# Optimization experiments

Hardware: AMD Instinct MI355X
Metric: run time of the kernel (lower is better)

The kernel has to match this reference:

```python
import jax, jax.numpy as jnp
import numpy as np

OUT_FEATURES = 11008
IN_FEATURES = 4096
GROUP_SIZE = 128
N_GROUPS = IN_FEATURES // GROUP_SIZE


def setup_inputs() -> dict:
    key = jax.random.key(0)
    k1, k2, k3 = jax.random.split(key, 3)
    x = jax.random.normal(k1, (4, 2048, IN_FEATURES), dtype=jnp.float32)
    # random packed bytes: every uint8 pattern decodes to a valid (low, high) nibble pair
    weight_packed = jax.random.randint(k2, (OUT_FEATURES, IN_FEATURES // 2), 0, 256, dtype=jnp.int32)
    # positive per-group scales (typical magnitude ~ max|w|/7)
    scales = jax.random.uniform(k3, (OUT_FEATURES, N_GROUPS), dtype=jnp.float32, minval=1e-3, maxval=0.05)
    return {"x": x, "weight_packed": weight_packed, "scales": scales}


def _dequant(weight_packed, scales):
    # unpack nibbles: low nibble = even index, high nibble = odd index; stored as (q+8)
    even = (weight_packed & 15) - 8                    # [O, I/2]
    odd = ((weight_packed >> 4) & 15) - 8              # [O, I/2]
    w_q = jnp.stack([even, odd], axis=-1).reshape(OUT_FEATURES, IN_FEATURES)  # interleave
    w = w_q.astype(jnp.float32).reshape(OUT_FEATURES, N_GROUPS, GROUP_SIZE)
    w = w * scales[:, :, None]                          # group-wise dequant
    return w.reshape(OUT_FEATURES, IN_FEATURES)


def reference(x, weight_packed, scales):
    w = _dequant(weight_packed, scales).astype(x.dtype)  # [O, I]
    # F.linear(x, w) = x @ w.T
    return jnp.einsum('bsi,oi->bso', x, w)
```

## Files before the change

kernel.cpp:

```cpp
#include <hip/hip_runtime.h>
#include <stdint.h>

#define K_DIM 4096
#define N_GROUPS 32

#define BM 128
#define BN 128
#define BK 32

#define BM8 256
#define BN8 256
#define BK8 64
#define NT8 (K_DIM / BK8)

typedef __attribute__((ext_vector_type(4))) float f32x4;
typedef __attribute__((ext_vector_type(8))) __bf16 bf16x8;
typedef __attribute__((ext_vector_type(4))) unsigned int u32x4;

__device__ __forceinline__ unsigned short f2bf(float f) {
    union { float f; unsigned u; } c; c.f = f;
    unsigned u = c.u;
    u += 0x7FFFu + ((u >> 16) & 1u);
    return (unsigned short)(u >> 16);
}

__global__ __launch_bounds__(256) void cvt_x(const float* __restrict__ x,
                                             unsigned short* __restrict__ xb,
                                             int total) {
    int i = (blockIdx.x * 256 + threadIdx.x) * 8;
    if (i >= total) return;
    f32x4 a = *(const f32x4*)(x + i);
    f32x4 b = *(const f32x4*)(x + i + 4);
    union { unsigned short u[8]; uint4 v; } o;
    o.u[0] = f2bf(a.x); o.u[1] = f2bf(a.y); o.u[2] = f2bf(a.z); o.u[3] = f2bf(a.w);
    o.u[4] = f2bf(b.x); o.u[5] = f2bf(b.y); o.u[6] = f2bf(b.z); o.u[7] = f2bf(b.w);
    *(uint4*)(xb + i) = o.v;
}

__global__ __launch_bounds__(256) void dequant_w(const int* __restrict__ wp,
                                                 const float* __restrict__ sc,
                                                 unsigned short* __restrict__ wd,
                                                 int total4) {
    int idx = blockIdx.x * 256 + threadIdx.x;
    if (idx >= total4) return;
    const int4 v = ((const int4*)wp)[idx];
    int flat = idx << 2;
    int n = flat >> 11;
    int ci = flat & 2047;
    float s = sc[(n << 5) + (ci >> 6)];
    union { unsigned short u[8]; uint4 q; } o;
    int vv[4] = { v.x, v.y, v.z, v.w };
#pragma unroll
    for (int j = 0; j < 4; ++j) {
        int e = (vv[j] & 15) - 8;
        int d = ((vv[j] >> 4) & 15) - 8;
        o.u[2 * j]     = f2bf((float)e * s);
        o.u[2 * j + 1] = f2bf((float)d * s);
    }
    *(uint4*)(wd + ((size_t)n << 12) + (ci << 1)) = o.q;
}

__device__ __forceinline__ void gld16(const void* g, void* l) {
    __builtin_amdgcn_global_load_lds((__attribute__((address_space(1))) void*)g,
                                     (__attribute__((address_space(3))) void*)l,
                                     16, 0, 0);
}

__device__ __forceinline__ bf16x8 dsr(unsigned a) {
    u32x4 d;
    asm volatile("ds_read_b128 %0, %1" : "=v"(d) : "v"(a));
    union { u32x4 u; bf16x8 b; } c; c.u = d;
    return c.b;
}

__device__ __forceinline__ unsigned lds_addr(const void* p) {
    return (unsigned)(uintptr_t)(__attribute__((address_space(3))) const void*)p;
}

#define MFMA_(va, vb, vc) __builtin_amdgcn_mfma_f32_16x16x32_bf16(va, vb, vc, 0, 0, 0)

#define STAGE(regbase, g, k) do {                                   \
    gld16((g) + (k), (regbase));                                    \
    gld16((g) + (size_t)128 * K_DIM + (k), (regbase) + 4096); } while (0)

__global__ __launch_bounds__(512, 2) void gemm8p(const unsigned short* __restrict__ A,
                                                 const unsigned short* __restrict__ B,
                                                 float* __restrict__ C,
                                                 int M, int N) {
    __shared__ __align__(16) unsigned short lds[2][4][8192];

    const int tid  = threadIdx.x;
    const int wave = tid >> 6;
    const int lane = tid & 63;
    const int wm = wave >> 2;
    const int wn = wave & 3;

    const int nwg = gridDim.x;
    const int bid = blockIdx.x;
    const int q = nwg >> 3, r7 = nwg & 7;
    const int xcd = bid & 7, loc = bid >> 3;
    const int tile = (xcd < r7 ? xcd * (q + 1) : r7 * (q + 1) + (xcd - r7) * q) + loc;
    const int ntm = M / BM8;
    const int tm = tile % ntm;
    const int tn = tile / ntm;
    const int m0 = tm * BM8;
    const int n0 = tn * BN8;

    const int srow = lane >> 2;
    const int sx   = ((lane & 3) * 8) ^ (((lane >> 3) & 3) << 3);
    const unsigned short* Ag = A + (size_t)(m0 + wave * 16 + srow) * K_DIM + sx;
    const unsigned short* Bg = B + (size_t)(n0 + wave * 16 + srow) * K_DIM + sx;
    unsigned short* L  = &lds[0][0][0];
    unsigned short* Ld = L + wave * 512;

    const int fr = lane & 15;
    const unsigned rofs = (unsigned)(fr * 64 + (((lane >> 4) * 16) ^ (((fr >> 1) & 3) << 4)));
    const unsigned ldsb = lds_addr(L);
    const unsigned aoff = ldsb + (unsigned)(wm * 8192) + rofs;
    const unsigned boff = ldsb + 32768u + (unsigned)(wn * 4096) + rofs;

    f32x4 acc[8][4] = {};
    bf16x8 a0[4], a1[4], b0[4], b1[4];

    STAGE(Ld + 0 * 8192, Ag, 0);
    STAGE(Ld + 1 * 8192, Ag, 32);
    STAGE(Ld + 2 * 8192, Bg, 0);
    STAGE(Ld + 3 * 8192, Bg, 32);
    STAGE(Ld + 32768 + 2 * 8192, Bg, 64);
    STAGE(Ld + 32768 + 0 * 8192, Ag, 64);
    STAGE(Ld + 32768 + 3 * 8192, Bg, 96);
    asm volatile("s_waitcnt vmcnt(6)" ::: "memory");
    __builtin_amdgcn_s_barrier();

    for (int T = 0; T < NT8; ++T) {
        const int buf = T & 1;
        const unsigned ab = aoff + (unsigned)(buf * 65536);
        const unsigned bb = boff + (unsigned)(buf * 65536);
        unsigned short* Lc = Ld + buf * 32768;
        unsigned short* Ln = Ld + (buf ^ 1) * 32768;
        const int kn1 = ((T + 1) < NT8 ? (T + 1) : NT8 - 1) * BK8;
        const int kn2 = ((T + 2) < NT8 ? (T + 2) : NT8 - 1) * BK8;

#pragma unroll
        for (int i = 0; i < 4; ++i) a0[i] = dsr(ab + i * 1024u);
#pragma unroll
        for (int j = 0; j < 4; ++j) b0[j] = dsr(bb + j * 1024u);
        STAGE(Ln + 1 * 8192, Ag, kn1 + 32);
        __builtin_amdgcn_s_barrier();
        asm volatile("s_waitcnt lgkmcnt(0)" ::: "memory");
        __builtin_amdgcn_sched_barrier(0);
        __builtin_amdgcn_s_setprio(1);
#pragma unroll
        for (int i = 0; i < 4; ++i)
#pragma unroll
            for (int j = 0; j < 4; ++j)
                acc[i][j] = MFMA_(a0[i], b0[j], acc[i][j]);
        __builtin_amdgcn_s_setprio(0);
        __builtin_amdgcn_s_barrier();

#pragma unroll
        for (int i = 0; i < 4; ++i) a1[i] = dsr(ab + (4 + i) * 1024u);
        STAGE(Lc + 2 * 8192, Bg, kn2);
        __builtin_amdgcn_s_barrier();
        asm volatile("s_waitcnt lgkmcnt(0)" ::: "memory");
        __builtin_amdgcn_sched_barrier(0);
        __builtin_amdgcn_s_setprio(1);
#pragma unroll
        for (int i = 0; i < 4; ++i)
#pragma unroll
            for (int j = 0; j < 4; ++j)
                acc[4 + i][j] = MFMA_(a1[i], b0[j], acc[4 + i][j]);
        __builtin_amdgcn_s_setprio(0);
        __builtin_amdgcn_s_barrier();

#pragma unroll
        for (int i = 0; i < 4; ++i) a0[i] = dsr(ab + 16384u + i * 1024u);
#pragma unroll
        for (int j = 0; j < 4; ++j) b1[j] = dsr(bb + 16384u + j * 1024u);
        STAGE(Lc + 0 * 8192, Ag, kn2);
        __builtin_amdgcn_s_barrier();
        asm volatile("s_waitcnt lgkmcnt(0)" ::: "memory");
        __builtin_amdgcn_sched_barrier(0);
        __builtin_amdgcn_s_setprio(1);
#pragma unroll
        for (int i = 0; i < 4; ++i)
#pragma unroll
            for (int j = 0; j < 4; ++j)
                acc[i][j] = MFMA_(a0[i], b1[j], acc[i][j]);
        __builtin_amdgcn_s_setprio(0);
        __builtin_amdgcn_s_barrier();

#pragma unroll
        for (int i = 0; i < 4; ++i) a1[i] = dsr(ab + 16384u + (4 + i) * 1024u);
        STAGE(Lc + 3 * 8192, Bg, kn2 + 32);
        __builtin_amdgcn_s_barrier();
        asm volatile("s_waitcnt lgkmcnt(0)" ::: "memory");
        __builtin_amdgcn_sched_barrier(0);
        __builtin_amdgcn_s_setprio(1);
#pragma unroll
        for (int i = 0; i < 4; ++i)
#pragma unroll
            for (int j = 0; j < 4; ++j)
                acc[4 + i][j] = MFMA_(a1[i], b1[j], acc[4 + i][j]);
        __builtin_amdgcn_s_setprio(0);
        asm volatile("s_waitcnt vmcnt(6)" ::: "memory");
        __builtin_amdgcn_s_barrier();
    }

    const int cr = (lane >> 4) * 4;
    const int cc = lane & 15;
#pragma unroll
    for (int i = 0; i < 8; ++i) {
#pragma unroll
        for (int j = 0; j < 4; ++j) {
            float* cp = C + (size_t)(m0 + wm * 128 + i * 16 + cr) * N + (n0 + wn * 64 + j * 16 + cc);
            cp[0]           = acc[i][j].x;
            cp[(size_t)N]   = acc[i][j].y;
            cp[(size_t)N*2] = acc[i][j].z;
            cp[(size_t)N*3] = acc[i][j].w;
        }
    }
}

__global__ __launch_bounds__(256, 2) void fused_gemm(const float* __restrict__ X,
                                                     const int* __restrict__ Wp,
                                                     const float* __restrict__ Sc,
                                                     float* __restrict__ C,
                                                     int M, int N) {
    __shared__ __align__(16) unsigned short As[BM * BK];
    __shared__ __align__(16) unsigned short Bs[BN * BK];

    const int tid  = threadIdx.x;
    const int wave = tid >> 6;
    const int lane = tid & 63;
    const int m0 = blockIdx.y * BM;
    const int n0 = blockIdx.x * BN;
    const int wm = (wave >> 1) * 64;
    const int wn = (wave & 1) * 64;

    const int fr = lane & 15;
    const int fk = (lane >> 4) * 8;

    f32x4 acc[4][4] = {};

    for (int k0 = 0; k0 < K_DIM; k0 += BK) {
        __syncthreads();
#pragma unroll
        for (int j = 0; j < 4; ++j) {
            int f = tid + 256 * j;
            int row = f >> 3, c4 = f & 7;
            f32x4 a = *(const f32x4*)(X + (size_t)(m0 + row) * K_DIM + k0 + c4 * 4);
            union { unsigned short u[4]; uint2 q; } o;
            o.u[0] = f2bf(a.x); o.u[1] = f2bf(a.y); o.u[2] = f2bf(a.z); o.u[3] = f2bf(a.w);
            *(uint2*)(As + row * BK + c4 * 4) = o.q;
        }
#pragma unroll
        for (int j = 0; j < 2; ++j) {
            int g = tid + 256 * j;
            int row = g >> 2, c4 = g & 3;
            const int4 v = *(const int4*)(Wp + (size_t)(n0 + row) * (K_DIM / 2) + (k0 >> 1) + c4 * 4);
            float s = Sc[(n0 + row) * N_GROUPS + (k0 >> 7)];
            union { unsigned short u[8]; uint4 q; } o;
            int vv[4] = { v.x, v.y, v.z, v.w };
#pragma unroll
            for (int t = 0; t < 4; ++t) {
                o.u[2 * t]     = f2bf((float)((vv[t] & 15) - 8) * s);
                o.u[2 * t + 1] = f2bf((float)(((vv[t] >> 4) & 15) - 8) * s);
            }
            *(uint4*)(Bs + row * BK + c4 * 8) = o.q;
        }
        __syncthreads();

        bf16x8 af[4], bf[4];
#pragma unroll
        for (int i = 0; i < 4; ++i) {
            af[i] = *(const bf16x8*)(As + (wm + i * 16 + fr) * BK + fk);
            bf[i] = *(const bf16x8*)(Bs + (wn + i * 16 + fr) * BK + fk);
        }
#pragma unroll
        for (int i = 0; i < 4; ++i)
#pragma unroll
            for (int j = 0; j < 4; ++j)
                acc[i][j] = __builtin_amdgcn_mfma_f32_16x16x32_bf16(af[i], bf[j], acc[i][j], 0, 0, 0);
    }

    const int cr = (lane >> 4) * 4;
    const int cc = lane & 15;
#pragma unroll
    for (int i = 0; i < 4; ++i) {
#pragma unroll
        for (int j = 0; j < 4; ++j) {
            float* cp = C + (size_t)(m0 + wm + i * 16 + cr) * N + (n0 + wn + j * 16 + cc);
            cp[0]           = acc[i][j].x;
            cp[(size_t)N]   = acc[i][j].y;
            cp[(size_t)N*2] = acc[i][j].z;
            cp[(size_t)N*3] = acc[i][j].w;
        }
    }
}

extern "C" void kernel_launch(void* const* d_in, const int* in_sizes, int n_in,
                              void* d_out, int out_size, void* d_ws, size_t ws_size,
                              hipStream_t stream) {
    const float* x  = (const float*)d_in[0];
    const int*   wp = (const int*)d_in[1];
    const float* sc = (const float*)d_in[2];
    float* out = (float*)d_out;

    const int M = in_sizes[0] / K_DIM;
    const int N = in_sizes[2] / N_GROUPS;

    const size_t xb_bytes = (size_t)M * K_DIM * 2;
    const size_t wd_bytes = (size_t)N * K_DIM * 2;

    const bool div256 = (M % BM8 == 0) && (N % BN8 == 0);

    if (ws_size >= xb_bytes + wd_bytes && div256) {
        unsigned short* xb = (unsigned short*)d_ws;
        unsigned short* wd = (unsigned short*)((char*)d_ws + xb_bytes);
        int xtot = M * K_DIM;
        cvt_x<<<xtot / (256 * 8), 256, 0, stream>>>(x, xb, xtot);
        int wtot4 = N * (K_DIM / 2) / 4;
        dequant_w<<<(wtot4 + 255) / 256, 256, 0, stream>>>(wp, sc, wd, wtot4);
        gemm8p<<<(M / BM8) * (N / BN8), 512, 0, stream>>>(xb, wd, out, M, N);
    } else {
        dim3 grid(N / BN, M / BM);
        fused_gemm<<<grid, 256, 0, stream>>>(x, wp, sc, out, M, N);
    }
}
```

Baseline: 1.238 ms.

## Software-pipeline LDS fragment reads ahead of each MFMA block

Restructures the main loop so each phase issues the LDS reads for the next phase's A/B fragments before running the current MFMA block. The next tile's first fragments are prefetched at the end of each iteration, and one barrier per phase is dropped. Reads now use immediate offsets in ds_read_b128 instead of per-read address arithmetic. This overlaps LDS latency with matrix math. The cost is more live registers and weaker synchronisation: the next buffer is read after only this thread's vmcnt wait, with no barrier to ensure other waves' async loads have landed.

```diff
diff --git a/kernel.cpp b/kernel.cpp
--- a/kernel.cpp
+++ b/kernel.cpp
@@ -66,12 +66,19 @@
                                      16, 0, 0);
 }
 
-__device__ __forceinline__ bf16x8 dsr(unsigned a) {
+template<int OFF>
+__device__ __forceinline__ bf16x8 dsrT(unsigned a) {
     u32x4 d;
-    asm volatile("ds_read_b128 %0, %1" : "=v"(d) : "v"(a));
+    asm volatile("ds_read_b128 %0, %1 offset:%2" : "=v"(d) : "v"(a), "n"(OFF));
     union { u32x4 u; bf16x8 b; } c; c.u = d;
     return c.b;
 }
+
+#define RD4(dst, base, o) do {              \
+    dst[0] = dsrT<(o)>(base);               \
+    dst[1] = dsrT<(o) + 1024>(base);        \
+    dst[2] = dsrT<(o) + 2048>(base);        \
+    dst[3] = dsrT<(o) + 3072>(base); } while (0)
 
 __device__ __forceinline__ unsigned lds_addr(const void* p) {
     return (unsigned)(uintptr_t)(__attribute__((address_space(3))) const void*)p;
@@ -132,22 +139,24 @@
     asm volatile("s_waitcnt vmcnt(6)" ::: "memory");
     __builtin_amdgcn_s_barrier();
 
+    RD4(a0, aoff, 0);
+    RD4(b0, boff, 0);
+
     for (int T = 0; T < NT8; ++T) {
         const int buf = T & 1;
-        const unsigned ab = aoff + (unsigned)(buf * 65536);
-        const unsigned bb = boff + (unsigned)(buf * 65536);
+        const unsigned ab  = aoff + (unsigned)(buf * 65536);
+        const unsigned bb  = boff + (unsigned)(buf * 65536);
+        const unsigned abn = ab ^ 65536u;
+        const unsigned bbn = bb ^ 65536u;
         unsigned short* Lc = Ld + buf * 32768;
         unsigned short* Ln = Ld + (buf ^ 1) * 32768;
         const int kn1 = ((T + 1) < NT8 ? (T + 1) : NT8 - 1) * BK8;
         const int kn2 = ((T + 2) < NT8 ? (T + 2) : NT8 - 1) * BK8;
 
-#pragma unroll
-        for (int i = 0; i < 4; ++i) a0[i] = dsr(ab + i * 1024u);
-#pragma unroll
-        for (int j = 0; j < 4; ++j) b0[j] = dsr(bb + j * 1024u);
+        asm volatile("s_waitcnt lgkmcnt(0)" ::: "memory");
+        __builtin_amdgcn_sched_barrier(0);
         STAGE(Ln + 1 * 8192, Ag, kn1 + 32);
-        __builtin_amdgcn_s_barrier();
-        asm volatile("s_waitcnt lgkmcnt(0)" ::: "memory");
+        RD4(a1, ab, 4096);
         __builtin_amdgcn_sched_barrier(0);
         __builtin_amdgcn_s_setprio(1);
 #pragma unroll
@@ -158,11 +167,11 @@
         __builtin_amdgcn_s_setprio(0);
         __builtin_amdgcn_s_barrier();
 
-#pragma unroll
-        for (int i = 0; i < 4; ++i) a1[i] = dsr(ab + (4 + i) * 1024u);
+        asm volatile("s_waitcnt lgkmcnt(0)" ::: "memory");
+        __builtin_amdgcn_sched_barrier(0);
         STAGE(Lc + 2 * 8192, Bg, kn2);
-        __builtin_amdgcn_s_barrier();
-        asm volatile("s_waitcnt lgkmcnt(0)" ::: "memory");
+        RD4(a0, ab, 16384);
+        RD4(b1, bb, 16384);
         __builtin_amdgcn_sched_barrier(0);
         __builtin_amdgcn_s_setprio(1);
 #pragma unroll
@@ -173,13 +182,10 @@
         __builtin_amdgcn_s_setprio(0);
         __builtin_amdgcn_s_barrier();
 
-#pragma unroll
-        for (int i = 0; i < 4; ++i) a0[i] = dsr(ab + 16384u + i * 1024u);
-#pragma unroll
-        for (int j = 0; j < 4; ++j) b1[j] = dsr(bb + 16384u + j * 1024u);
+        asm volatile("s_waitcnt lgkmcnt(0)" ::: "memory");
+        __builtin_amdgcn_sched_barrier(0);
         STAGE(Lc + 0 * 8192, Ag, kn2);
-        __builtin_amdgcn_s_barrier();
-        asm volatile("s_waitcnt lgkmcnt(0)" ::: "memory");
+        RD4(a1, ab, 16384 + 4096);
         __builtin_amdgcn_sched_barrier(0);
         __builtin_amdgcn_s_setprio(1);
 #pragma unroll
@@ -190,11 +196,12 @@
         __builtin_amdgcn_s_setprio(0);
         __builtin_amdgcn_s_barrier();
 
-#pragma unroll
-        for (int i = 0; i < 4; ++i) a1[i] = dsr(ab + 16384u + (4 + i) * 1024u);
+        asm volatile("s_waitcnt lgkmcnt(0)" ::: "memory");
+        __builtin_amdgcn_sched_barrier(0);
         STAGE(Lc + 3 * 8192, Bg, kn2 + 32);
-        __builtin_amdgcn_s_barrier();
-        asm volatile("s_waitcnt lgkmcnt(0)" ::: "memory");
+        asm volatile("s_waitcnt vmcnt(6)" ::: "memory");
+        RD4(a0, abn, 0);
+        RD4(b0, bbn, 0);
         __builtin_amdgcn_sched_barrier(0);
         __builtin_amdgcn_s_setprio(1);
 #pragma unroll
@@ -203,7 +210,6 @@
             for (int j = 0; j < 4; ++j)
                 acc[4 + i][j] = MFMA_(a1[i], b1[j], acc[4 + i][j]);
         __builtin_amdgcn_s_setprio(0);
-        asm volatile("s_waitcnt vmcnt(6)" ::: "memory");
         __builtin_amdgcn_s_barrier();
     }
 
```

Measured after the change: 1.274 ms. 2.9% more time.
